# Optimization experiments

Hardware: AMD Instinct MI355X
Metric: run time of the kernel (lower is better)

Reference implementation:

```python
import jax, jax.numpy as jnp
import numpy as np

NUM_CENTROIDS = 64
NUM_KMEANS = 5
KM_ITERS = 20


def _kmeans_labels(X, key):
    """Lloyd k-means on X [N,D]; returns final cluster labels [N] (int32).
    Mirrors faiss.Kmeans(dim, num_centroids, niter=...) label assignment."""
    N, D = X.shape
    idx = jax.random.choice(key, N, (NUM_CENTROIDS,), replace=False)
    cent0 = X[idx]  # [C,D] init from random data points

    def assign(cent):
        d = (cent * cent).sum(-1)[None, :] - 2.0 * (X @ cent.T)  # [N,C]
        return jnp.argmin(d, axis=1)

    def step(cent, _):
        lab = assign(cent)
        sums = jax.ops.segment_sum(X, lab, num_segments=NUM_CENTROIDS)  # [C,D]
        cnts = jax.ops.segment_sum(jnp.ones((N,), X.dtype), lab, num_segments=NUM_CENTROIDS)
        newc = jnp.where(cnts[:, None] > 0, sums / jnp.maximum(cnts, 1.0)[:, None], cent)
        return newc, None

    cent, _ = jax.lax.scan(step, cent0, None, length=KM_ITERS)
    return assign(cent)


def setup_inputs() -> dict:
    key = jax.random.key(0)
    k1, k2, k3 = jax.random.split(key, 3)
    N, D = 8192, 512
    adj = jax.random.uniform(k1, (N, N), dtype=jnp.float32)
    student = jax.random.normal(k2, (N, D), dtype=jnp.float32)
    teacher = jax.random.normal(k3, (N, D), dtype=jnp.float32)
    return {"adj": adj, "student": student, "teacher": teacher, "topk": 16}


def reference(adj, student, teacher, topk):
    N, D = student.shape
    # similarity = (student @ teacher.T).detach() + 10*I
    sim = jax.lax.stop_gradient(student @ teacher.T) + 10.0 * jnp.eye(N, dtype=student.dtype)
    _, I_knn = jax.lax.top_k(sim, topk)  # [N, k], sorted descending
    rows = jnp.arange(N)[:, None]  # [N,1]

    # knn_neighbor: sparse ones at (row, I_knn); topk cols are distinct per row
    knn_pat = jnp.zeros((N, N), adj.dtype).at[rows, I_knn].set(1.0)
    locality = knn_pat * adj  # sparse elementwise product knn_neighbor * adj

    # k-means cluster labels over NUM_KMEANS seeds (teacher is detached/cpu in torch)
    Xt = jax.lax.stop_gradient(teacher)
    keys = jax.random.split(jax.random.key(1234), NUM_KMEANS)
    labels = jax.vmap(lambda k: _kmeans_labels(Xt, k))(keys)  # [M,N]

    # close-in-background mask: any seed where label(i) == label(knn_j(i))
    ngh_lab = labels[:, I_knn]               # [M,N,k]
    mask = jnp.any(labels[:, :, None] == ngh_lab, axis=0)  # [N,k]

    # globality: ones at masked (row, knn) positions
    glob_pat = jnp.zeros((N, N), adj.dtype).at[rows, I_knn].add(mask.astype(adj.dtype))

    # pos = locality + globality (dense equivalent of coalesced sparse sum)
    pos = locality + glob_pat
    return pos
```

## Files before the change

kernel.cpp:

```cpp
#include <hip/hip_runtime.h>
#include <stdint.h>

typedef unsigned int u32;
typedef unsigned long long u64;
typedef __attribute__((ext_vector_type(8))) short short8;
typedef __attribute__((ext_vector_type(4))) float f32x4;

#define NN 8192
#define DD 512
#define CC 64
#define RR 5
#define KM_ITERS 20
#define TOPKK 16
#define CHUNK 8192
#define GAP_TH 0.05f
#define FLAGTH 0.02f
#define BAND_TH 0.01f
#define FIXCAP (RR * NN)

#define MFMA_BF16 __builtin_amdgcn_mfma_f32_16x16x32_bf16

__device__ __forceinline__ void gload16(void* lds, const void* g) {
  __builtin_amdgcn_global_load_lds(
      (const __attribute__((address_space(1))) void*)g,
      (__attribute__((address_space(3))) void*)lds, 16, 0, 0);
}

__device__ __forceinline__ void tf2x32(u32 k0, u32 k1, u32 x0, u32 x1,
                                       u32& o0, u32& o1) {
  u32 ks2 = k0 ^ k1 ^ 0x1BD11BDAu;
  x0 += k0; x1 += k1;
#define TFR(r) { x0 += x1; x1 = (x1 << r) | (x1 >> (32 - r)); x1 ^= x0; }
  TFR(13) TFR(15) TFR(26) TFR(6)
  x0 += k1; x1 += ks2 + 1u;
  TFR(17) TFR(29) TFR(16) TFR(24)
  x0 += ks2; x1 += k0 + 2u;
  TFR(13) TFR(15) TFR(26) TFR(6)
  x0 += k0; x1 += k1 + 3u;
  TFR(17) TFR(29) TFR(16) TFR(24)
  x0 += k1; x1 += ks2 + 4u;
  TFR(13) TFR(15) TFR(26) TFR(6)
  x0 += ks2; x1 += k0 + 5u;
#undef TFR
  o0 = x0; o1 = x1;
}

__global__ __launch_bounds__(256) void rng_kernel(u32* __restrict__ bits1,
                                                  u32* __restrict__ bits2) {
  int r = blockIdx.x;
  int i = blockIdx.y * 256 + threadIdx.x;
  u32 rk0, rk1; tf2x32(0u, 1234u, 0u, (u32)r, rk0, rk1);
  u32 k10, k11, s10, s11, s20, s21;
  tf2x32(rk0, rk1, 0u, 0u, k10, k11);
  tf2x32(rk0, rk1, 0u, 1u, s10, s11);
  tf2x32(k10, k11, 0u, 1u, s20, s21);
  u32 a, b;
  tf2x32(s10, s11, 0u, (u32)i, a, b);
  bits1[r * NN + i] = a ^ b;
  tf2x32(s20, s21, 0u, (u32)i, a, b);
  bits2[r * NN + i] = a ^ b;
}

__global__ __launch_bounds__(256) void rankpart_kernel(const u32* __restrict__ bits,
                                                       u32* __restrict__ prank) {
  __shared__ u64 sk[2048];
  int r = blockIdx.x, zc = blockIdx.z;
  const u32* bb = bits + (size_t)r * NN;
  int jbase = zc * 2048;
  for (int t = threadIdx.x; t < 2048; t += 256)
    sk[t] = ((u64)bb[jbase + t] << 13) | (u32)(jbase + t);
  __syncthreads();
  int i = blockIdx.y * 256 + threadIdx.x;
  u64 ki = ((u64)bb[i] << 13) | (u32)i;
  int cnt = 0;
#pragma unroll 8
  for (int j = 0; j < 2048; ++j) cnt += (int)(sk[j] < ki);
  prank[(size_t)(r * 4 + zc) * NN + i] = cnt;
}

__global__ __launch_bounds__(256) void scat1_kernel(const u32* __restrict__ prank,
                                                    int* __restrict__ vout) {
  int r = blockIdx.x;
  int i = blockIdx.y * 256 + threadIdx.x;
  int rank = prank[(size_t)(r * 4 + 0) * NN + i] + prank[(size_t)(r * 4 + 1) * NN + i] +
             prank[(size_t)(r * 4 + 2) * NN + i] + prank[(size_t)(r * 4 + 3) * NN + i];
  vout[(size_t)r * NN + rank] = i;
}

__global__ __launch_bounds__(256) void scat2_kernel(const u32* __restrict__ prank,
                                                    const int* __restrict__ v1,
                                                    int* __restrict__ sel) {
  int r = blockIdx.x;
  int i = blockIdx.y * 256 + threadIdx.x;
  int rank = prank[(size_t)(r * 4 + 0) * NN + i] + prank[(size_t)(r * 4 + 1) * NN + i] +
             prank[(size_t)(r * 4 + 2) * NN + i] + prank[(size_t)(r * 4 + 3) * NN + i];
  if (rank < CC) sel[r * CC + rank] = v1[(size_t)r * NN + i];
}

__device__ __forceinline__ double block_reduce_d(double s, double* red4) {
  int tid = threadIdx.x;
  for (int off = 32; off > 0; off >>= 1) s += __shfl_down(s, off, 64);
  if ((tid & 63) == 0) red4[tid >> 6] = s;
  __syncthreads();
  return red4[0] + red4[1] + red4[2] + red4[3];
}

__device__ __forceinline__ u32 bf16rne(float a) {
  u32 ab = __float_as_uint(a);
  return (ab + 0x7FFFu + ((ab >> 16) & 1u)) >> 16;
}
__device__ __forceinline__ void splitf(float a, unsigned short& hi, unsigned short& lo) {
  u32 h = bf16rne(a);
  float hf = __uint_as_float(h << 16);
  hi = (unsigned short)h;
  lo = (unsigned short)bf16rne(a - hf);
}

__global__ __launch_bounds__(256) void init_cent_kernel(const float* __restrict__ X,
                                                        const int* __restrict__ sel,
                                                        double* __restrict__ centD,
                                                        double* __restrict__ cnD,
                                                        float* __restrict__ cnF,
                                                        unsigned short* __restrict__ CHg,
                                                        unsigned short* __restrict__ CLg) {
  __shared__ double red4[4];
  int r = blockIdx.x, c = blockIdx.y, t = threadIdx.x;
  int src = sel[r * CC + c];
  const float* xp = X + (size_t)src * DD;
  size_t o = (size_t)(r * CC + c) * DD;
  double va = (double)xp[t], vb = (double)xp[t + 256];
  centD[o + t] = va; centD[o + t + 256] = vb;
  unsigned short h0, l0, h1, l1;
  splitf((float)va, h0, l0); splitf((float)vb, h1, l1);
  CHg[o + t] = h0; CLg[o + t] = l0;
  CHg[o + t + 256] = h1; CLg[o + t + 256] = l1;
  double tot = block_reduce_d(va * va + vb * vb, red4);
  if (t == 0) { cnD[r * CC + c] = tot; cnF[r * CC + c] = (float)tot; }
}

__global__ __launch_bounds__(256) void split_kernel(const float* __restrict__ in,
                                                    unsigned short* __restrict__ hi,
                                                    unsigned short* __restrict__ lo) {
  size_t base = ((size_t)blockIdx.x * 256 + threadIdx.x) * 8;
  float4 v0 = *(const float4*)(in + base);
  float4 v1 = *(const float4*)(in + base + 4);
  float vv[8] = {v0.x, v0.y, v0.z, v0.w, v1.x, v1.y, v1.z, v1.w};
  unsigned short h[8], l[8];
#pragma unroll
  for (int j = 0; j < 8; ++j) splitf(vv[j], h[j], l[j]);
  uint4 hv, lv;
  hv.x = h[0] | ((u32)h[1] << 16); hv.y = h[2] | ((u32)h[3] << 16);
  hv.z = h[4] | ((u32)h[5] << 16); hv.w = h[6] | ((u32)h[7] << 16);
  lv.x = l[0] | ((u32)l[1] << 16); lv.y = l[2] | ((u32)l[3] << 16);
  lv.z = l[4] | ((u32)l[5] << 16); lv.w = l[6] | ((u32)l[7] << 16);
  *(uint4*)(hi + base) = hv;
  *(uint4*)(lo + base) = lv;
}

__global__ __launch_bounds__(256) void assign_kernel(const unsigned short* __restrict__ XH,
                                                     const unsigned short* __restrict__ XL,
                                                     const unsigned short* __restrict__ CHg,
                                                     const unsigned short* __restrict__ CLg,
                                                     const float* __restrict__ cnF,
                                                     int* __restrict__ labels,
                                                     u32* __restrict__ flags,
                                                     u32* __restrict__ counter) {
  __shared__ unsigned short Xh[2 * 64 * 32], Xl[2 * 64 * 32],
                            Ch[2 * 64 * 32], Cl[2 * 64 * 32];
  __shared__ float dmat[64 * 68];
  int r = blockIdx.y;
  int blk = blockIdx.x;
  int rowBase = blk * 64;
  int tid = threadIdx.x;
  int wid = tid >> 6, lane = tid & 63, m = lane & 15, q = lane >> 4;
  int srow = wid * 16 + (lane >> 2);
  int sslot = (lane & 3) * 8;
  const unsigned short* gxh = XH + (size_t)(rowBase + srow) * DD + sslot;
  const unsigned short* gxl = XL + (size_t)(rowBase + srow) * DD + sslot;
  const unsigned short* gch = CHg + ((size_t)r * CC + srow) * DD + sslot;
  const unsigned short* gcl = CLg + ((size_t)r * CC + srow) * DD + sslot;
  f32x4 acc[4] = {};
  for (int kc = 0; kc < DD; kc += 64) {
#pragma unroll
    for (int p = 0; p < 2; ++p) {
      int off = p * 2048, ko = kc + p * 32;
      gload16(&Xh[off + wid * 512], gxh + ko);
      gload16(&Xl[off + wid * 512], gxl + ko);
      gload16(&Ch[off + wid * 512], gch + ko);
      gload16(&Cl[off + wid * 512], gcl + ko);
    }
    __syncthreads();
#pragma unroll
    for (int s = 0; s < 2; ++s) {
      int off = s * 2048;
      short8 ah = *(short8*)&Xh[off + (wid * 16 + m) * 32 + q * 8];
      short8 al = *(short8*)&Xl[off + (wid * 16 + m) * 32 + q * 8];
#pragma unroll
      for (int nt = 0; nt < 4; ++nt) {
        short8 bh = *(short8*)&Ch[off + (nt * 16 + m) * 32 + q * 8];
        short8 bl = *(short8*)&Cl[off + (nt * 16 + m) * 32 + q * 8];
        acc[nt] = MFMA_BF16(ah, bh, acc[nt], 0, 0, 0);
        acc[nt] = MFMA_BF16(ah, bl, acc[nt], 0, 0, 0);
        acc[nt] = MFMA_BF16(al, bh, acc[nt], 0, 0, 0);
      }
    }
    __syncthreads();
  }
#pragma unroll
  for (int nt = 0; nt < 4; ++nt) {
    float cn = cnF[r * CC + nt * 16 + m];
#pragma unroll
    for (int reg = 0; reg < 4; ++reg)
      dmat[(wid * 16 + q * 4 + reg) * 68 + nt * 16 + m] = cn - 2.0f * acc[nt][reg];
  }
  __syncthreads();
  if (tid < 64) {
    const float* dr = dmat + (size_t)tid * 68;
    float best = dr[0], second = 3.4e38f; int bi = 0;
    for (int c = 1; c < CC; ++c) {
      float v = dr[c];
      if (v < best) { second = best; best = v; bi = c; }
      else if (v < second) second = v;
    }
    labels[(size_t)r * NN + rowBase + tid] = bi;
    if (second - best < GAP_TH) {
      u32 idx = atomicAdd(counter, 1u);
      if (idx < FIXCAP) flags[idx] = (u32)(r * NN + rowBase + tid);
    }
  }
}

__global__ __launch_bounds__(256) void fixup_kernel(const float* __restrict__ X,
                                                    const double* __restrict__ centD,
                                                    const double* __restrict__ cnD,
                                                    const u32* __restrict__ flags,
                                                    const u32* __restrict__ counter,
                                                    int* __restrict__ labels) {
  __shared__ double darr[CC];
  int n = (int)*counter; if (n > FIXCAP) n = FIXCAP;
  int tid = threadIdx.x, c = tid >> 2, sub = tid & 3;
  for (int f = blockIdx.x; f < n; f += gridDim.x) {
    u32 pk = flags[f];
    int r = pk >> 13, i = pk & (NN - 1);
    const float* x = X + (size_t)i * DD + sub * 128;
    const double* cp = centD + (size_t)(r * CC + c) * DD + sub * 128;
    double s = 0.0;
    for (int k = 0; k < 128; ++k) s += (double)x[k] * cp[k];
    s += __shfl_down(s, 2, 64);
    s += __shfl_down(s, 1, 64);
    if (sub == 0) darr[c] = cnD[r * CC + c] - 2.0 * s;
    __syncthreads();
    if (tid == 0) {
      double best = darr[0]; int bi = 0;
      for (int cc = 1; cc < CC; ++cc) { double v = darr[cc]; if (v < best) { best = v; bi = cc; } }
      labels[(size_t)r * NN + i] = bi;
    }
    __syncthreads();
  }
}

__global__ __launch_bounds__(64) void hist_kernel(const int* __restrict__ labels,
                                                  int* __restrict__ bhist,
                                                  int* __restrict__ rib) {
  __shared__ int labs[64];
  __shared__ int h[CC];
  int r = blockIdx.y, blk = blockIdx.x, tid = threadIdx.x;
  labs[tid] = labels[(size_t)r * NN + blk * 64 + tid];
  h[tid] = 0;
  __syncthreads();
  int lab = labs[tid];
  atomicAdd(&h[lab], 1);
  int rk = 0;
  for (int j = 0; j < tid; ++j) rk += (labs[j] == lab);
  rib[(size_t)r * NN + blk * 64 + tid] = rk;
  __syncthreads();
  bhist[(size_t)(r * 128 + blk) * CC + tid] = h[tid];
}

__global__ __launch_bounds__(256) void fill_kernel(const int* __restrict__ labels,
                                                   const int* __restrict__ rib,
                                                   const int* __restrict__ bhist,
                                                   int* __restrict__ cstart,
                                                   int* __restrict__ cnt,
                                                   int* __restrict__ member) {
  __shared__ int bh[128 * CC];
  __shared__ int cs[CC];
  __shared__ int tots[CC];
  int r = blockIdx.x, blk = blockIdx.y, tid = threadIdx.x;
  const int* src = bhist + (size_t)r * 128 * CC;
  for (int t = tid; t < 128 * CC; t += 256) bh[t] = src[t];
  __syncthreads();
  if (tid < CC) {
    int run = 0;
    for (int b = 0; b < 128; ++b) { int v = bh[b * CC + tid]; bh[b * CC + tid] = run; run += v; }
    tots[tid] = run;
  }
  __syncthreads();
  if (tid == 0) {
    int run = 0;
    for (int q2 = 0; q2 < CC; ++q2) { cs[q2] = run; run += tots[q2]; }
  }
  __syncthreads();
  int i = blk * 256 + tid;
  int lab = labels[(size_t)r * NN + i];
  int pos = cs[lab] + bh[(i >> 6) * CC + lab] + rib[(size_t)r * NN + i];
  member[(size_t)r * NN + pos] = i;
  if (blk == 0 && tid < CC) { cnt[r * CC + tid] = tots[tid]; cstart[r * CC + tid] = cs[tid]; }
}

__global__ __launch_bounds__(256) void update_kernel(const float* __restrict__ X,
                                                     const int* __restrict__ member,
                                                     const int* __restrict__ cstart,
                                                     const int* __restrict__ cnt,
                                                     const double* __restrict__ centOld,
                                                     double* __restrict__ centNew) {
  __shared__ double part[4][64];
  int r = blockIdx.x, c = blockIdx.y, dchunk = blockIdx.z;
  int tid = threadIdx.x;
  int d = dchunk * 64 + (tid & 63);
  int lane = tid >> 6;
  int n = cnt[r * CC + c];
  int st = cstart[r * CC + c];
  const int* mem = member + (size_t)r * NN + st;
  int n4 = (n + 3) >> 2;
  int lo = lane * n4;
  int hi = min(n, lo + n4);
  double s0 = 0, s1 = 0, s2 = 0, s3 = 0;
  int m = lo;
  for (; m + 3 < hi; m += 4) {
    s0 += (double)X[(size_t)mem[m + 0] * DD + d];
    s1 += (double)X[(size_t)mem[m + 1] * DD + d];
    s2 += (double)X[(size_t)mem[m + 2] * DD + d];
    s3 += (double)X[(size_t)mem[m + 3] * DD + d];
  }
  for (; m < hi; ++m) s0 += (double)X[(size_t)mem[m] * DD + d];
  part[lane][tid & 63] = (s0 + s1) + (s2 + s3);
  __syncthreads();
  if (tid < 64) {
    double tot = (part[0][tid] + part[1][tid]) + (part[2][tid] + part[3][tid]);
    size_t o = (size_t)(r * CC + c) * DD + dchunk * 64 + tid;
    double va = (n > 0) ? tot / (double)n : centOld[o];
    centNew[o] = va;
  }
}

__global__ __launch_bounds__(256) void norm_kernel(const double* __restrict__ centNew,
                                                   double* __restrict__ cnD,
                                                   float* __restrict__ cnF,
                                                   unsigned short* __restrict__ CHg,
                                                   unsigned short* __restrict__ CLg) {
  __shared__ double red4[4];
  int r = blockIdx.x, c = blockIdx.y, t = threadIdx.x;
  size_t o = (size_t)(r * CC + c) * DD;
  double va = centNew[o + t], vb = centNew[o + t + 256];
  unsigned short h0, l0, h1, l1;
  splitf((float)va, h0, l0); splitf((float)vb, h1, l1);
  CHg[o + t] = h0; CLg[o + t] = l0;
  CHg[o + t + 256] = h1; CLg[o + t + 256] = l1;
  double tot = block_reduce_d(va * va + vb * vb, red4);
  if (t == 0) { cnD[r * CC + c] = tot; cnF[r * CC + c] = (float)tot; }
}

__global__ __launch_bounds__(256) void gemm_kernel(const unsigned short* __restrict__ SH,
                                                   const unsigned short* __restrict__ SL,
                                                   const unsigned short* __restrict__ TH,
                                                   const unsigned short* __restrict__ TL,
                                                   float* __restrict__ sim,
                                                   int rowChunk) {
  __shared__ unsigned short Ah[2 * 128 * 32], Al[2 * 128 * 32],
                            Bh[2 * 128 * 32], Bl[2 * 128 * 32];
  int tid = threadIdx.x;
  int wid = tid >> 6, lane = tid & 63, m = lane & 15, q = lane >> 4;
  int waveM = wid >> 1, waveN = wid & 1;
  const int nwgx = NN / 128;
  const int nwg = nwgx * (CHUNK / 128);
  int wg = blockIdx.y * nwgx + blockIdx.x;
  int swz = (wg & 7) * (nwg >> 3) + (wg >> 3);
  int rowTile = swz / nwgx, colTile = swz % nwgx;
  int rowBase = rowChunk + rowTile * 128;
  int colBase = colTile * 128;
  int sr0 = wid * 16 + (lane >> 2);
  int sr1 = (wid + 4) * 16 + (lane >> 2);
  int sslot = (lane & 3) * 8;
  const unsigned short* gah0 = SH + (size_t)(rowBase + sr0) * DD + sslot;
  const unsigned short* gah1 = SH + (size_t)(rowBase + sr1) * DD + sslot;
  const unsigned short* gal0 = SL + (size_t)(rowBase + sr0) * DD + sslot;
  const unsigned short* gal1 = SL + (size_t)(rowBase + sr1) * DD + sslot;
  const unsigned short* gbh0 = TH + (size_t)(colBase + sr0) * DD + sslot;
  const unsigned short* gbh1 = TH + (size_t)(colBase + sr1) * DD + sslot;
  const unsigned short* gbl0 = TL + (size_t)(colBase + sr0) * DD + sslot;
  const unsigned short* gbl1 = TL + (size_t)(colBase + sr1) * DD + sslot;
  f32x4 acc[4][4] = {};
  for (int kc = 0; kc < DD; kc += 64) {
#pragma unroll
    for (int p = 0; p < 2; ++p) {
      int off = p * 4096, ko = kc + p * 32;
      gload16(&Ah[off + wid * 512], gah0 + ko);
      gload16(&Ah[off + (wid + 4) * 512], gah1 + ko);
      gload16(&Al[off + wid * 512], gal0 + ko);
      gload16(&Al[off + (wid + 4) * 512], gal1 + ko);
      gload16(&Bh[off + wid * 512], gbh0 + ko);
      gload16(&Bh[off + (wid + 4) * 512], gbh1 + ko);
      gload16(&Bl[off + wid * 512], gbl0 + ko);
      gload16(&Bl[off + (wid + 4) * 512], gbl1 + ko);
    }
    __syncthreads();
#pragma unroll
    for (int s = 0; s < 2; ++s) {
      int off = s * 4096;
      short8 ah[4], al[4], bh[4], bl[4];
#pragma unroll
      for (int t = 0; t < 4; ++t) {
        ah[t] = *(short8*)&Ah[off + (waveM * 64 + t * 16 + m) * 32 + q * 8];
        al[t] = *(short8*)&Al[off + (waveM * 64 + t * 16 + m) * 32 + q * 8];
        bh[t] = *(short8*)&Bh[off + (waveN * 64 + t * 16 + m) * 32 + q * 8];
        bl[t] = *(short8*)&Bl[off + (waveN * 64 + t * 16 + m) * 32 + q * 8];
      }
#pragma unroll
      for (int mt = 0; mt < 4; ++mt)
#pragma unroll
        for (int nt = 0; nt < 4; ++nt) {
          acc[mt][nt] = MFMA_BF16(ah[mt], bh[nt], acc[mt][nt], 0, 0, 0);
          acc[mt][nt] = MFMA_BF16(ah[mt], bl[nt], acc[mt][nt], 0, 0, 0);
          acc[mt][nt] = MFMA_BF16(al[mt], bh[nt], acc[mt][nt], 0, 0, 0);
        }
    }
    __syncthreads();
  }
#pragma unroll
  for (int mt = 0; mt < 4; ++mt)
#pragma unroll
    for (int nt = 0; nt < 4; ++nt) {
      int gcol = colBase + waveN * 64 + nt * 16 + m;
#pragma unroll
      for (int reg = 0; reg < 4; ++reg) {
        int lrow = rowTile * 128 + waveM * 64 + mt * 16 + q * 4 + reg;
        int grow = rowChunk + lrow;
        float v = acc[mt][nt][reg];
        if (grow == gcol) v += 10.0f;
        sim[(size_t)lrow * NN + gcol] = v;
      }
    }
}

__global__ __launch_bounds__(256) void topk_kernel(const float* __restrict__ sim,
                                                   const float* __restrict__ S,
                                                   const float* __restrict__ T,
                                                   int* __restrict__ iknn,
                                                   int rowChunk) {
  __shared__ u32 rowk[NN];
  __shared__ int bins[4096];
  __shared__ int partial[256];
  __shared__ u64 cand[128];
  __shared__ u64 sure[40];
  __shared__ u64 outk[TOPKK + 1];
  __shared__ u64 red[4];
  __shared__ int nsure, ncand, selB1, selB2, needSel, hardcase;
  __shared__ int nsureR, nbandR;
  __shared__ int sidx[16];
  __shared__ int bidx[64];
  __shared__ double bval[64];

  int blk = blockIdx.x, tid = threadIdx.x;
  int grow = rowChunk + blk;
  const float* rp = sim + (size_t)blk * NN;

  for (int t = tid; t < 4096; t += 256) bins[t] = 0;
  if (tid == 0) { nsure = 0; ncand = 0; hardcase = 0; }
  __syncthreads();
  for (int t = tid; t < NN; t += 256) {
    u32 u = __float_as_uint(rp[t]);
    u = (u & 0x80000000u) ? ~u : (u | 0x80000000u);
    rowk[t] = u;
    atomicAdd(&bins[u >> 20], 1);
  }
  __syncthreads();
  int ps = 0;
#pragma unroll
  for (int b = 0; b < 16; ++b) ps += bins[tid * 16 + b];
  partial[tid] = ps;
  __syncthreads();
  if (tid == 0) {
    int cum = 0, c = 255;
    for (; c > 0; --c) { if (cum + partial[c] >= 17) break; cum += partial[c]; }
    int b = c * 16 + 15;
    for (; b > c * 16; --b) { if (cum + bins[b] >= 17) break; cum += bins[b]; }
    selB1 = b; needSel = 17 - cum;
  }
  __syncthreads();
  int B1 = selB1;
  for (int t = tid; t < NN; t += 256) {
    u32 u = rowk[t];
    int b = (int)(u >> 20);
    if (b < B1) continue;
    u64 key = ((u64)u << 32) | (u32)(NN - 1 - t);
    if (b > B1) { int s = atomicAdd(&nsure, 1); if (s < 40) sure[s] = key; else hardcase = 1; }
    else        { int s = atomicAdd(&ncand, 1); if (s < 128) cand[s] = key; }
  }
  __syncthreads();
  if (ncand > 128) {
    for (int t = tid; t < 4096; t += 256) bins[t] = 0;
    __syncthreads();
    for (int t = tid; t < NN; t += 256) {
      u32 u = rowk[t];
      if ((int)(u >> 20) == B1) atomicAdd(&bins[(u >> 8) & 0xFFFu], 1);
    }
    __syncthreads();
    int p2 = 0;
#pragma unroll
    for (int b = 0; b < 16; ++b) p2 += bins[tid * 16 + b];
    partial[tid] = p2;
    __syncthreads();
    if (tid == 0) {
      int need = needSel;
      int cum = 0, c = 255;
      for (; c > 0; --c) { if (cum + partial[c] >= need) break; cum += partial[c]; }
      int b = c * 16 + 15;
      for (; b > c * 16; --b) { if (cum + bins[b] >= need) break; cum += bins[b]; }
      selB2 = b; ncand = 0;
    }
    __syncthreads();
    int B2 = selB2;
    for (int t = tid; t < NN; t += 256) {
      u32 u = rowk[t];
      if ((int)(u >> 20) != B1) continue;
      int sb = (int)((u >> 8) & 0xFFFu);
      if (sb < B2) continue;
      u64 key = ((u64)u << 32) | (u32)(NN - 1 - t);
      if (sb > B2) { int s = atomicAdd(&nsure, 1); if (s < 40) sure[s] = key; else hardcase = 1; }
      else         { int s = atomicAdd(&ncand, 1); if (s < 128) cand[s] = key; }
    }
    __syncthreads();
    if (tid == 0 && ncand > 128) hardcase = 1;
    __syncthreads();
  }
  if (!hardcase) {
    int ns = nsure, nc = ncand;
    int total = ns + nc;
    if (tid < total) {
      u64 k = tid < ns ? sure[tid] : cand[tid - ns];
      int rank = 0;
      for (int j = 0; j < total; ++j) {
        u64 o = j < ns ? sure[j] : cand[j - ns];
        rank += (int)(o > k);
      }
      if (rank < TOPKK + 1) outk[rank] = k;
    }
  } else {
    for (int k = 0; k < TOPKK + 1; ++k) {
      u64 best = 0;
      for (int t = tid; t < NN; t += 256) {
        u64 key = ((u64)rowk[t] << 32) | (u32)(NN - 1 - t);
        best = key > best ? key : best;
      }
      for (int off = 32; off > 0; off >>= 1) {
        u32 lo = (u32)best, hi = (u32)(best >> 32);
        lo = __shfl_down(lo, off, 64); hi = __shfl_down(hi, off, 64);
        u64 o = ((u64)hi << 32) | lo;
        best = o > best ? o : best;
      }
      if ((tid & 63) == 0) red[tid >> 6] = best;
      __syncthreads();
      if (tid == 0) {
        u64 b = red[0];
        for (int w = 1; w < 4; ++w) b = red[w] > b ? red[w] : b;
        outk[k] = b;
        rowk[(NN - 1) - (int)(b & 0xFFFFFFFFu)] = 0;
      }
      __syncthreads();
    }
  }
  __syncthreads();
  if (hardcase && tid < TOPKK + 1) {
    u64 k = outk[tid];
    rowk[(NN - 1) - (int)(k & 0xFFFFFFFFu)] = (u32)(k >> 32);
  }
  __syncthreads();
  if (tid < TOPKK)
    iknn[(size_t)grow * TOPKK + tid] = (NN - 1) - (int)(outk[tid] & 0xFFFFFFFFu);
  u32 ub16 = (u32)(outk[TOPKK - 1] >> 32), ub17 = (u32)(outk[TOPKK] >> 32);
  float v16 = (ub16 & 0x80000000u) ? __uint_as_float(ub16 & 0x7FFFFFFFu)
                                   : __uint_as_float(~ub16);
  float v17 = (ub17 & 0x80000000u) ? __uint_as_float(ub17 & 0x7FFFFFFFu)
                                   : __uint_as_float(~ub17);
  if (v16 - v17 >= FLAGTH) return;

  if (tid == 0) { nsureR = 0; nbandR = 0; }
  __syncthreads();
  for (int j = tid; j < NN; j += 256) {
    u32 u = rowk[j];
    float v = (u & 0x80000000u) ? __uint_as_float(u & 0x7FFFFFFFu)
                                : __uint_as_float(~u);
    if (v > v16 + BAND_TH) {
      int s = atomicAdd(&nsureR, 1);
      if (s < 16) sidx[s] = j;
    } else if (v >= v16 - BAND_TH) {
      int s = atomicAdd(&nbandR, 1);
      if (s < 64) bidx[s] = j;
    }
  }
  __syncthreads();
  int nb = nbandR > 64 ? 64 : nbandR;
  if (tid < nb) {
    const float* sp = S + (size_t)grow * DD;
    const float* tp = T + (size_t)bidx[tid] * DD;
    double s = 0.0;
    for (int k = 0; k < DD; ++k) s += (double)sp[k] * (double)tp[k];
    bval[tid] = s;
  }
  __syncthreads();
  if (tid == 0) {
    int w = 0;
    int ns = nsureR < 16 ? nsureR : 16;
    for (int i2 = 0; i2 < ns; ++i2) iknn[(size_t)grow * TOPKK + w++] = sidx[i2];
    u64 used = 0;
    while (w < TOPKK) {
      int bj = -1; double bv = 0.0;
      for (int i2 = 0; i2 < nb; ++i2) {
        if (used & (1ull << i2)) continue;
        if (bj < 0 || bval[i2] > bv ||
            (bval[i2] == bv && bidx[i2] < bidx[bj])) { bv = bval[i2]; bj = i2; }
      }
      if (bj < 0) break;
      used |= 1ull << bj;
      iknn[(size_t)grow * TOPKK + w++] = bidx[bj];
    }
  }
}

__global__ __launch_bounds__(256) void zero_kernel(float4* __restrict__ out) {
  size_t i = (size_t)blockIdx.x * 256 + threadIdx.x;
  out[i] = make_float4(0.f, 0.f, 0.f, 0.f);
}

__global__ void zeroc_kernel(u32* __restrict__ c) {
  c[threadIdx.x] = 0u;
}

__global__ __launch_bounds__(256) void scatter_kernel(const float* __restrict__ adj,
                                                      const int* __restrict__ iknn,
                                                      const int* __restrict__ labels,
                                                      float* __restrict__ out) {
  int idx = blockIdx.x * 256 + threadIdx.x;
  int i = idx >> 4;
  int col = iknn[idx];
  int m = 0;
#pragma unroll
  for (int r = 0; r < RR; ++r)
    m |= (labels[(size_t)r * NN + i] == labels[(size_t)r * NN + col]);
  size_t o = (size_t)i * NN + col;
  out[o] = adj[o] + (float)m;
}

extern "C" void kernel_launch(void* const* d_in, const int* in_sizes, int n_in,
                              void* d_out, int out_size, void* d_ws, size_t ws_size,
                              hipStream_t stream) {
  (void)in_sizes; (void)n_in; (void)out_size; (void)ws_size;
  const float* adj     = (const float*)d_in[0];
  const float* student = (const float*)d_in[1];
  const float* teacher = (const float*)d_in[2];
  float* out = (float*)d_out;

  char* p = (char*)d_ws;
  auto alloc = [&](size_t bytes) -> void* {
    void* q = (void*)p; p += (bytes + 255) & ~(size_t)255; return q;
  };
  double* centA  = (double*)alloc((size_t)RR * CC * DD * 8);
  double* centB  = (double*)alloc((size_t)RR * CC * DD * 8);
  double* cnD    = (double*)alloc((size_t)RR * CC * 8);
  float*  cnF    = (float*) alloc((size_t)RR * CC * 4);
  u32*    bits1  = (u32*)   alloc((size_t)RR * NN * 4);
  u32*    bits2  = (u32*)   alloc((size_t)RR * NN * 4);
  u32*    prank  = (u32*)   alloc((size_t)RR * 4 * NN * 4);
  int*    v1     = (int*)   alloc((size_t)RR * NN * 4);
  int*    sel    = (int*)   alloc((size_t)RR * CC * 4);
  int*    labels = (int*)   alloc((size_t)RR * NN * 4);
  int*    bhist  = (int*)   alloc((size_t)RR * 128 * CC * 4);
  int*    cstart = (int*)   alloc((size_t)RR * CC * 4);
  int*    cnt    = (int*)   alloc((size_t)RR * CC * 4);
  int*    rib    = (int*)   alloc((size_t)RR * NN * 4);
  int*    member = (int*)   alloc((size_t)RR * NN * 4);
  u32*    flags  = (u32*)   alloc((size_t)FIXCAP * 4);
  u32*    counters = (u32*) alloc((size_t)64 * 4);
  int*    iknn   = (int*)   alloc((size_t)NN * TOPKK * 4);
  unsigned short* SH = (unsigned short*)alloc((size_t)NN * DD * 2);
  unsigned short* SL = (unsigned short*)alloc((size_t)NN * DD * 2);
  unsigned short* THi = (unsigned short*)alloc((size_t)NN * DD * 2);
  unsigned short* TLo = (unsigned short*)alloc((size_t)NN * DD * 2);
  unsigned short* CHg = (unsigned short*)alloc((size_t)RR * CC * DD * 2);
  unsigned short* CLg = (unsigned short*)alloc((size_t)RR * CC * DD * 2);
  float*  simc   = (float*) alloc((size_t)CHUNK * NN * 4);

  zeroc_kernel<<<1, 64, 0, stream>>>(counters);

  rng_kernel<<<dim3(RR, 32), 256, 0, stream>>>(bits1, bits2);
  rankpart_kernel<<<dim3(RR, 32, 4), 256, 0, stream>>>(bits1, prank);
  scat1_kernel<<<dim3(RR, 32), 256, 0, stream>>>(prank, v1);
  rankpart_kernel<<<dim3(RR, 32, 4), 256, 0, stream>>>(bits2, prank);
  scat2_kernel<<<dim3(RR, 32), 256, 0, stream>>>(prank, v1, sel);
  init_cent_kernel<<<dim3(RR, CC), 256, 0, stream>>>(teacher, sel, centA, cnD, cnF, CHg, CLg);

  split_kernel<<<(NN * DD / 8) / 256, 256, 0, stream>>>(student, SH, SL);
  split_kernel<<<(NN * DD / 8) / 256, 256, 0, stream>>>(teacher, THi, TLo);

  double* cur = centA; double* nxt = centB;
  for (int it = 0; it < KM_ITERS; ++it) {
    assign_kernel<<<dim3(NN / 64, RR), 256, 0, stream>>>(THi, TLo, CHg, CLg, cnF,
                                                         labels, flags, counters + it);
    fixup_kernel<<<1024, 256, 0, stream>>>(teacher, cur, cnD, flags, counters + it, labels);
    hist_kernel<<<dim3(128, RR), 64, 0, stream>>>(labels, bhist, rib);
    fill_kernel<<<dim3(RR, 32), 256, 0, stream>>>(labels, rib, bhist, cstart, cnt, member);
    update_kernel<<<dim3(RR, CC, 8), 256, 0, stream>>>(teacher, member, cstart, cnt, cur, nxt);
    norm_kernel<<<dim3(RR, CC), 256, 0, stream>>>(nxt, cnD, cnF, CHg, CLg);
    double* t = cur; cur = nxt; nxt = t;
  }
  assign_kernel<<<dim3(NN / 64, RR), 256, 0, stream>>>(THi, TLo, CHg, CLg, cnF,
                                                       labels, flags, counters + KM_ITERS);
  fixup_kernel<<<1024, 256, 0, stream>>>(teacher, cur, cnD, flags,
                                         counters + KM_ITERS, labels);

  gemm_kernel<<<dim3(NN / 128, CHUNK / 128), 256, 0, stream>>>(SH, SL, THi, TLo, simc, 0);
  topk_kernel<<<CHUNK, 256, 0, stream>>>(simc, student, teacher, iknn, 0);

  zero_kernel<<<(unsigned)((size_t)NN * NN / 4 / 256), 256, 0, stream>>>((float4*)out);
  scatter_kernel<<<NN * TOPKK / 256, 256, 0, stream>>>(adj, iknn, labels, out);
}
```

Measured before the change: 2.699 ms.

## Bin top-k on float values, drop LDS row copy, chunk similarity GEMM

The top-k kernel no longer copies each 8192-wide row into shared memory. It histograms values directly into linear 0.125-wide bins and re-reads the row from global memory, which should hit in cache. The second-level refinement pass is removed, and the rare overflow case is handled by a brute-force arg-max that excludes already chosen keys. The similarity GEMM and top-k now run over two 4096-row chunks, halving the scratch buffer so it has a better chance of staying in L2 or last-level cache. The trade-offs are extra global re-reads and a fixed bin range, so values outside ±256 are clamped and may push more rows into the slow path.

```diff
diff --git a/kernel.cpp b/kernel.cpp
--- a/kernel.cpp
+++ b/kernel.cpp
@@ -12,11 +12,13 @@
 #define RR 5
 #define KM_ITERS 20
 #define TOPKK 16
-#define CHUNK 8192
+#define CHUNK 4096
 #define GAP_TH 0.05f
 #define FLAGTH 0.02f
 #define BAND_TH 0.01f
 #define FIXCAP (RR * NN)
+#define TK_LO 256.0f
+#define TK_SCALE 8.0f
 
 #define MFMA_BF16 __builtin_amdgcn_mfma_f32_16x16x32_bf16
 
@@ -24,6 +26,15 @@
   __builtin_amdgcn_global_load_lds(
       (const __attribute__((address_space(1))) void*)g,
       (__attribute__((address_space(3))) void*)lds, 16, 0, 0);
+}
+
+__device__ __forceinline__ u32 keyenc(float v) {
+  u32 u = __float_as_uint(v);
+  return (u & 0x80000000u) ? ~u : (u | 0x80000000u);
+}
+__device__ __forceinline__ int tkbin(float v) {
+  int b = (int)((v + TK_LO) * TK_SCALE);
+  return b < 0 ? 0 : (b > 4095 ? 4095 : b);
 }
 
 __device__ __forceinline__ void tf2x32(u32 k0, u32 k1, u32 x0, u32 x1,
@@ -448,14 +459,13 @@
                                                    const float* __restrict__ T,
                                                    int* __restrict__ iknn,
                                                    int rowChunk) {
-  __shared__ u32 rowk[NN];
   __shared__ int bins[4096];
   __shared__ int partial[256];
   __shared__ u64 cand[128];
-  __shared__ u64 sure[40];
+  __shared__ u64 sure[24];
   __shared__ u64 outk[TOPKK + 1];
   __shared__ u64 red[4];
-  __shared__ int nsure, ncand, selB1, selB2, needSel, hardcase;
+  __shared__ int nsure, ncand, selB1, hardcase;
   __shared__ int nsureR, nbandR;
   __shared__ int sidx[16];
   __shared__ int bidx[64];
@@ -468,12 +478,7 @@
   for (int t = tid; t < 4096; t += 256) bins[t] = 0;
   if (tid == 0) { nsure = 0; ncand = 0; hardcase = 0; }
   __syncthreads();
-  for (int t = tid; t < NN; t += 256) {
-    u32 u = __float_as_uint(rp[t]);
-    u = (u & 0x80000000u) ? ~u : (u | 0x80000000u);
-    rowk[t] = u;
-    atomicAdd(&bins[u >> 20], 1);
-  }
+  for (int t = tid; t < NN; t += 256) atomicAdd(&bins[tkbin(rp[t])], 1);
   __syncthreads();
   int ps = 0;
 #pragma unroll
@@ -485,55 +490,21 @@
     for (; c > 0; --c) { if (cum + partial[c] >= 17) break; cum += partial[c]; }
     int b = c * 16 + 15;
     for (; b > c * 16; --b) { if (cum + bins[b] >= 17) break; cum += bins[b]; }
-    selB1 = b; needSel = 17 - cum;
+    selB1 = b;
   }
   __syncthreads();
   int B1 = selB1;
   for (int t = tid; t < NN; t += 256) {
-    u32 u = rowk[t];
-    int b = (int)(u >> 20);
+    float v = rp[t];
+    int b = tkbin(v);
     if (b < B1) continue;
-    u64 key = ((u64)u << 32) | (u32)(NN - 1 - t);
-    if (b > B1) { int s = atomicAdd(&nsure, 1); if (s < 40) sure[s] = key; else hardcase = 1; }
+    u64 key = ((u64)keyenc(v) << 32) | (u32)(NN - 1 - t);
+    if (b > B1) { int s = atomicAdd(&nsure, 1); if (s < 24) sure[s] = key; }
     else        { int s = atomicAdd(&ncand, 1); if (s < 128) cand[s] = key; }
   }
   __syncthreads();
-  if (ncand > 128) {
-    for (int t = tid; t < 4096; t += 256) bins[t] = 0;
-    __syncthreads();
-    for (int t = tid; t < NN; t += 256) {
-      u32 u = rowk[t];
-      if ((int)(u >> 20) == B1) atomicAdd(&bins[(u >> 8) & 0xFFFu], 1);
-    }
-    __syncthreads();
-    int p2 = 0;
-#pragma unroll
-    for (int b = 0; b < 16; ++b) p2 += bins[tid * 16 + b];
-    partial[tid] = p2;
-    __syncthreads();
-    if (tid == 0) {
-      int need = needSel;
-      int cum = 0, c = 255;
-      for (; c > 0; --c) { if (cum + partial[c] >= need) break; cum += partial[c]; }
-      int b = c * 16 + 15;
-      for (; b > c * 16; --b) { if (cum + bins[b] >= need) break; cum += bins[b]; }
-      selB2 = b; ncand = 0;
-    }
-    __syncthreads();
-    int B2 = selB2;
-    for (int t = tid; t < NN; t += 256) {
-      u32 u = rowk[t];
-      if ((int)(u >> 20) != B1) continue;
-      int sb = (int)((u >> 8) & 0xFFFu);
-      if (sb < B2) continue;
-      u64 key = ((u64)u << 32) | (u32)(NN - 1 - t);
-      if (sb > B2) { int s = atomicAdd(&nsure, 1); if (s < 40) sure[s] = key; else hardcase = 1; }
-      else         { int s = atomicAdd(&ncand, 1); if (s < 128) cand[s] = key; }
-    }
-    __syncthreads();
-    if (tid == 0 && ncand > 128) hardcase = 1;
-    __syncthreads();
-  }
+  if (tid == 0 && ncand > 128) hardcase = 1;
+  __syncthreads();
   if (!hardcase) {
     int ns = nsure, nc = ncand;
     int total = ns + nc;
@@ -546,12 +517,15 @@
       }
       if (rank < TOPKK + 1) outk[rank] = k;
     }
+    __syncthreads();
   } else {
     for (int k = 0; k < TOPKK + 1; ++k) {
       u64 best = 0;
       for (int t = tid; t < NN; t += 256) {
-        u64 key = ((u64)rowk[t] << 32) | (u32)(NN - 1 - t);
-        best = key > best ? key : best;
+        u64 key = ((u64)keyenc(rp[t]) << 32) | (u32)(NN - 1 - t);
+        bool excl = false;
+        for (int j = 0; j < k; ++j) excl |= (outk[j] == key);
+        if (!excl && key > best) best = key;
       }
       for (int off = 32; off > 0; off >>= 1) {
         u32 lo = (u32)best, hi = (u32)(best >> 32);
@@ -565,17 +539,10 @@
         u64 b = red[0];
         for (int w = 1; w < 4; ++w) b = red[w] > b ? red[w] : b;
         outk[k] = b;
-        rowk[(NN - 1) - (int)(b & 0xFFFFFFFFu)] = 0;
       }
       __syncthreads();
     }
   }
-  __syncthreads();
-  if (hardcase && tid < TOPKK + 1) {
-    u64 k = outk[tid];
-    rowk[(NN - 1) - (int)(k & 0xFFFFFFFFu)] = (u32)(k >> 32);
-  }
-  __syncthreads();
   if (tid < TOPKK)
     iknn[(size_t)grow * TOPKK + tid] = (NN - 1) - (int)(outk[tid] & 0xFFFFFFFFu);
   u32 ub16 = (u32)(outk[TOPKK - 1] >> 32), ub17 = (u32)(outk[TOPKK] >> 32);
@@ -588,9 +555,7 @@
   if (tid == 0) { nsureR = 0; nbandR = 0; }
   __syncthreads();
   for (int j = tid; j < NN; j += 256) {
-    u32 u = rowk[j];
-    float v = (u & 0x80000000u) ? __uint_as_float(u & 0x7FFFFFFFu)
-                                : __uint_as_float(~u);
+    float v = rp[j];
     if (v > v16 + BAND_TH) {
       int s = atomicAdd(&nsureR, 1);
       if (s < 16) sidx[s] = j;
@@ -719,8 +684,11 @@
   fixup_kernel<<<1024, 256, 0, stream>>>(teacher, cur, cnD, flags,
                                          counters + KM_ITERS, labels);
 
-  gemm_kernel<<<dim3(NN / 128, CHUNK / 128), 256, 0, stream>>>(SH, SL, THi, TLo, simc, 0);
-  topk_kernel<<<CHUNK, 256, 0, stream>>>(simc, student, teacher, iknn, 0);
+  for (int ch = 0; ch < NN / CHUNK; ++ch) {
+    gemm_kernel<<<dim3(NN / 128, CHUNK / 128), 256, 0, stream>>>(SH, SL, THi, TLo, simc,
+                                                                 ch * CHUNK);
+    topk_kernel<<<CHUNK, 256, 0, stream>>>(simc, student, teacher, iknn, ch * CHUNK);
+  }
 
   zero_kernel<<<(unsigned)((size_t)NN * NN / 4 / 256), 256, 0, stream>>>((float4*)out);
   scatter_kernel<<<NN * TOPKK / 256, 256, 0, stream>>>(adj, iknn, labels, out);
```

Result: faster. 2.604 ms (-3.5%).
